# Kernel tuning notes

Measured on AMD Instinct MI355X. Metric: run time of the kernel, lower is better.

Reference implementation:

```python
import jax, jax.numpy as jnp
import numpy as np

# Keras GRUCell (reset_after=True, default in TF2) step
# Keras LSTMCell step (gate order i, f, c, o)
# Keras RNN masking semantics: at masked steps, states are frozen and the
# step output is the previous output (equivalent to freezing every layer's h).

def _gru_step(a, h, W, U, bi, br):
    gx = a @ W + bi          # [B, 3H] input projection
    gh = h @ U + br          # [B, 3H] recurrent projection (reset_after)
    xz, xr, xh = jnp.split(gx, 3, axis=-1)
    rz, rr, rh = jnp.split(gh, 3, axis=-1)
    z = jax.nn.sigmoid(xz + rz)
    r = jax.nn.sigmoid(xr + rr)
    hh = jnp.tanh(xh + r * rh)
    return z * h + (1.0 - z) * hh


def _lstm_step(a, h, c, W, U, b):
    g = a @ W + h @ U + b    # [B, 4H]
    gi, gf, gc, go = jnp.split(g, 4, axis=-1)
    i = jax.nn.sigmoid(gi)
    f = jax.nn.sigmoid(gf)
    cn = f * c + i * jnp.tanh(gc)
    hn = jax.nn.sigmoid(go) * jnp.tanh(cn)
    return hn, cn


def run_gru_stack(x, mask, layers):
    # x: [B,T,D], mask: [B,T] bool; layers: list of (W,U,bi,br)
    B = x.shape[0]
    H = layers[0][1].shape[0]
    xT = jnp.swapaxes(x, 0, 1)      # [T,B,D]
    mT = jnp.swapaxes(mask, 0, 1)   # [T,B]

    def step(hs, inp):
        xt, mt = inp
        a = xt
        new = []
        for (W, U, bi, br), h in zip(layers, hs):
            hn = _gru_step(a, h, W, U, bi, br)
            hn = jnp.where(mt[:, None], hn, h)  # freeze state under mask
            new.append(hn)
            a = hn
        return tuple(new), a

    h0 = tuple(jnp.zeros((B, H), x.dtype) for _ in layers)
    _, ys = jax.lax.scan(step, h0, (xT, mT))
    return jnp.swapaxes(ys, 0, 1)   # [B,T,H]


def run_lstm_stack(x, mask, layers):
    # layers: list of (W,U,b)
    B = x.shape[0]
    H = layers[0][1].shape[0]
    xT = jnp.swapaxes(x, 0, 1)
    mT = jnp.swapaxes(mask, 0, 1)

    def step(state, inp):
        xt, mt = inp
        a = xt
        new = []
        for (W, U, b), (h, c) in zip(layers, state):
            hn, cn = _lstm_step(a, h, c, W, U, b)
            hn = jnp.where(mt[:, None], hn, h)
            cn = jnp.where(mt[:, None], cn, c)
            new.append((hn, cn))
            a = hn
        return tuple(new), a

    s0 = tuple((jnp.zeros((B, H), x.dtype), jnp.zeros((B, H), x.dtype)) for _ in layers)
    _, ys = jax.lax.scan(step, s0, (xT, mT))
    return jnp.swapaxes(ys, 0, 1)


def _forward(x, lengths, g_W0, g_U0, g_bi0, g_br0, g_W1, g_U1, g_bi1, g_br1,
             l_W0, l_U0, l_b0, l_W1, l_U1, l_b1, out_W, out_b):
    T = x.shape[1]
    mask = jnp.arange(T)[None, :] < lengths[:, None]          # [B,T]
    o1 = run_gru_stack(x, mask, [(g_W0, g_U0, g_bi0, g_br0),
                                 (g_W1, g_U1, g_bi1, g_br1)])  # [B,T,H]
    o2 = run_lstm_stack(x, mask, [(l_W0, l_U0, l_b0),
                                  (l_W1, l_U1, l_b1)])          # [B,T,H]
    c = jnp.concatenate([o1, o2], axis=-1)                      # [B,T,2H]
    return c @ out_W + out_b                                    # [B,T,1]


def setup_inputs() -> dict:
    key = jax.random.key(0)
    ks = jax.random.split(key, 16)
    B, T, D, H = 64, 512, 96, 256
    glorot = lambda k, shp: (jax.random.normal(k, shp, dtype=jnp.float32)
                             / np.sqrt(shp[0]).astype(np.float32))
    inp = {
        "x": jax.random.normal(ks[0], (B, T, D), dtype=jnp.float32),
        "lengths": jax.random.randint(ks[1], (B,), 1, T + 1),
        # GRU stack (reset_after: separate input/recurrent biases)
        "g_W0": glorot(ks[2], (D, 3 * H)),
        "g_U0": glorot(ks[3], (H, 3 * H)),
        "g_bi0": jnp.zeros((3 * H,), jnp.float32),
        "g_br0": jnp.zeros((3 * H,), jnp.float32),
        "g_W1": glorot(ks[4], (H, 3 * H)),
        "g_U1": glorot(ks[5], (H, 3 * H)),
        "g_bi1": jnp.zeros((3 * H,), jnp.float32),
        "g_br1": jnp.zeros((3 * H,), jnp.float32),
        # LSTM stack
        "l_W0": glorot(ks[6], (D, 4 * H)),
        "l_U0": glorot(ks[7], (H, 4 * H)),
        "l_b0": jnp.zeros((4 * H,), jnp.float32),
        "l_W1": glorot(ks[8], (H, 4 * H)),
        "l_U1": glorot(ks[9], (H, 4 * H)),
        "l_b1": jnp.zeros((4 * H,), jnp.float32),
        # Dense head on concat [.., 2H] -> 1
        "out_W": glorot(ks[10], (2 * H, 1)),
        "out_b": jnp.zeros((1,), jnp.float32),
    }
    return inp


def reference(x, lengths, g_W0, g_U0, g_bi0, g_br0, g_W1, g_U1, g_bi1, g_br1,
              l_W0, l_U0, l_b0, l_W1, l_U1, l_b1, out_W, out_b):
    return _forward(x, lengths, g_W0, g_U0, g_bi0, g_br0, g_W1, g_U1, g_bi1,
                    g_br1, l_W0, l_U0, l_b0, l_W1, l_U1, l_b1, out_W, out_b)
```

## Files before the change

kernel.cpp:

```cpp
#include <hip/hip_runtime.h>
#include <hip/hip_fp16.h>

constexpr int Tt = 512, Dd = 96, Hh = 256;
constexpr int NS0 = 16;
constexpr int NSP = 8;
typedef unsigned long long u64;

constexpr size_t OFF_P0  = (size_t)4 << 20;
constexpr size_t OFF_P1  = (size_t)12 << 20;
constexpr size_t OFF_FLG = (size_t)20 << 20;
constexpr size_t OFF_W16 = ((size_t)20 << 20) + ((size_t)64 << 10);
constexpr size_t oGW0 = 0;
constexpr size_t oGU0 = oGW0 + (size_t)48 * 768;
constexpr size_t oGW1 = oGU0 + (size_t)128 * 768;
constexpr size_t oGU1 = oGW1 + (size_t)128 * 768;
constexpr size_t oLW0 = oGU1 + (size_t)128 * 768;
constexpr size_t oLU0 = oLW0 + (size_t)48 * 1024;
constexpr size_t oLW1 = oLU0 + (size_t)128 * 1024;
constexpr size_t oLU1 = oLW1 + (size_t)128 * 1024;

__device__ __forceinline__ float sigf(float v) { return 1.0f / (1.0f + __expf(-v)); }
__device__ __forceinline__ u64 agld(const u64* p) {
    return __hip_atomic_load(p, __ATOMIC_RELAXED, __HIP_MEMORY_SCOPE_AGENT);
}
__device__ __forceinline__ int agldi(const int* p) {
    return __hip_atomic_load(p, __ATOMIC_ACQUIRE, __HIP_MEMORY_SCOPE_AGENT);
}
__device__ __forceinline__ void agst(u64* p, u64 v) {
    __hip_atomic_store(p, v, __ATOMIC_RELAXED, __HIP_MEMORY_SCOPE_AGENT);
}

__device__ __forceinline__ float dot2f(unsigned w, unsigned a, float acc) {
#if __has_builtin(__builtin_amdgcn_fdot2)
    typedef _Float16 h2v __attribute__((ext_vector_type(2)));
    h2v wh, ah;
    __builtin_memcpy(&wh, &w, 4);
    __builtin_memcpy(&ah, &a, 4);
    return __builtin_amdgcn_fdot2(wh, ah, acc, false);
#else
    const float2 wf = __half22float2(*(const __half2*)&w);
    const float2 af = __half22float2(*(const __half2*)&a);
    acc = fmaf(wf.x, af.x, acc);
    return fmaf(wf.y, af.y, acc);
#endif
}

__device__ __forceinline__ int hidx(int k, int r) {
    return (k >> 1) * 8 + r * 2 + (k & 1);
}

template<int G>
__device__ __forceinline__ void load4h(uint4* wv, const uint4* __restrict__ M4,
                                       int ldm, int kpb) {
    const int base = (kpb >> 2) * ldm;
    #pragma unroll
    for (int g = 0; g < G; ++g)
        wv[g] = M4[base + g * 256];
}
template<int G>
__device__ __forceinline__ void fma4h(const uint4* wv, const uint4* __restrict__ A4,
                                      int kpb, float4* acc) {
    const uint4 a0 = A4[kpb + 0];
    const uint4 a1 = A4[kpb + 1];
    const uint4 a2 = A4[kpb + 2];
    const uint4 a3 = A4[kpb + 3];
    #pragma unroll
    for (int g = 0; g < G; ++g) {
        const uint4 w = wv[g];
        acc[g].x = dot2f(w.x, a0.x, acc[g].x);
        acc[g].y = dot2f(w.x, a0.y, acc[g].y);
        acc[g].z = dot2f(w.x, a0.z, acc[g].z);
        acc[g].w = dot2f(w.x, a0.w, acc[g].w);
        acc[g].x = dot2f(w.y, a1.x, acc[g].x);
        acc[g].y = dot2f(w.y, a1.y, acc[g].y);
        acc[g].z = dot2f(w.y, a1.z, acc[g].z);
        acc[g].w = dot2f(w.y, a1.w, acc[g].w);
        acc[g].x = dot2f(w.z, a2.x, acc[g].x);
        acc[g].y = dot2f(w.z, a2.y, acc[g].y);
        acc[g].z = dot2f(w.z, a2.z, acc[g].z);
        acc[g].w = dot2f(w.z, a2.w, acc[g].w);
        acc[g].x = dot2f(w.w, a3.x, acc[g].x);
        acc[g].y = dot2f(w.w, a3.y, acc[g].y);
        acc[g].z = dot2f(w.w, a3.z, acc[g].z);
        acc[g].w = dot2f(w.w, a3.w, acc[g].w);
    }
}
template<int G>
__device__ __forceinline__ void gemmP(const uint4* __restrict__ M4, int ldm,
                                      const uint4* __restrict__ A4,
                                      int kp0, int kp1, float4* acc) {
    const int n4 = (kp1 - kp0) >> 2;
    uint4 wv0[G], wv1[G];
    if (n4 <= 0) return;
    load4h<G>(wv0, M4, ldm, kp0);
    int c2 = 0;
    for (; c2 + 2 <= n4; c2 += 2) {
        load4h<G>(wv1, M4, ldm, kp0 + (c2 + 1) * 4);
        fma4h<G>(wv0, A4, kp0 + c2 * 4, acc);
        if (c2 + 2 < n4) load4h<G>(wv0, M4, ldm, kp0 + (c2 + 2) * 4);
        fma4h<G>(wv1, A4, kp0 + (c2 + 1) * 4, acc);
    }
    if (c2 < n4) fma4h<G>(wv0, A4, kp0 + c2 * 4, acc);
}

__global__ void cvt_pair(const float* __restrict__ src, unsigned* __restrict__ dst,
                         int n, int ld) {
    const int i = blockIdx.x * 256 + threadIdx.x;
    if (i >= n) return;
    const int kp = i / ld, col = i - kp * ld;
    const __half2 h = __floats2half2_rn(src[(2 * kp) * ld + col],
                                        src[(2 * kp + 1) * ld + col]);
    dst[((size_t)((kp >> 2) * ld + col) << 2) + (kp & 3)] = *(const unsigned*)&h;
}

__global__ void __launch_bounds__(1024, 4)
rnn_persist(const float* __restrict__ x, const int* __restrict__ lengths,
            const float* __restrict__ gbi0, const float* __restrict__ gbr0,
            const float* __restrict__ gbi1, const float* __restrict__ gbr1,
            const float* __restrict__ lb0, const float* __restrict__ lb1,
            const float* __restrict__ outW, const float* __restrict__ outb,
            float* __restrict__ out, char* __restrict__ wsb)
{
    const int tid = threadIdx.x;
    const int c   = tid & 255;
    const int grp = tid >> 8;
    const int bx  = blockIdx.x;
    const int role  = bx & 3;
    const int chain = (bx >> 2) & 1;
    const int rg    = bx >> 3;
    const int rowbase = rg * 4;

    const int GA  = chain ? 4 : 3;
    const int GAH = GA * Hh;

    u64* h0ring = (u64*)wsb + (size_t)(chain * 16 + rg) * (NS0 * 1024);
    u64* p0ring = (u64*)(wsb + OFF_P0) + (size_t)(chain * 16 + rg) * (NSP * 4096);
    u64* p1ring = (u64*)(wsb + OFF_P1) + (size_t)(chain * 16 + rg) * (NSP * 4096);
    int* flags = (int*)(wsb + OFF_FLG);
    int* flg_r0 = flags + ((chain * 16 + rg) * 4 + 1) * 32;
    int* flg_p1 = flags + ((chain * 16 + rg) * 4 + 2) * 32;
    int* flg_r1 = flags + ((chain * 16 + rg) * 4 + 3) * 32;

    const unsigned* W16 = (const unsigned*)(wsb + OFF_W16);
    size_t woff;
    if (chain == 0) woff = (role == 0) ? oGW0 : (role == 1) ? oGU0 : (role == 2) ? oGW1 : oGU1;
    else            woff = (role == 0) ? oLW0 : (role == 1) ? oLU0 : (role == 2) ? oLW1 : oLU1;
    const uint4* M4 = (const uint4*)(W16 + woff) + c;

    const int KR  = (role == 0) ? Dd : Hh;
    const int KP2 = KR >> 3;
    const int kp0 = grp * KP2, kp1 = kp0 + KP2;

    __shared__ __align__(16) unsigned sAh[128 * 4];
    __shared__ float sG[2 * 4096];
    __shared__ float sRed[16];
    __half* sAhh = (__half*)sAh;
    const uint4* A4 = (const uint4*)sAh;

    const int NP  = 4 * GAH;
    const int npt = NP >> 10;
    float biasv[4];
    int sgidx[4];
    if (role == 0 || role == 2) {
        const float* bsrc = (chain == 0) ? (role == 0 ? gbi0 : gbi1)
                                         : (role == 0 ? lb0 : lb1);
        #pragma unroll
        for (int i = 0; i < 4; ++i) {
            if (i < npt) {
                const int e = tid + i * 1024;
                const int r = e / GAH, rem = e - r * GAH;
                biasv[i] = bsrc[rem];
                sgidx[i] = r * 1024 + rem;
            } else { biasv[i] = 0; sgidx[i] = 0; }
        }
    }
    const int rA = grp;
    const int lenA = lengths[rowbase + rA];
    float brz = 0, brr = 0, brh = 0, ow = 0;
    if (chain == 0 && (role == 1 || role == 3)) {
        const float* br = (role == 1) ? gbr0 : gbr1;
        brz = br[c]; brr = br[Hh + c]; brh = br[2 * Hh + c];
    }
    if (role == 3) ow = outW[chain * Hh + c];
    const float outb0 = outb[0];
    float creg = 0.0f;
    float hprev = 0.0f;

    for (int i = tid; i < 512; i += 1024) sAh[i] = 0;
    __syncthreads();

    for (int t = 0; t < Tt; ++t) {
        if (role == 0) {
            if (t >= NSP) {
                if (tid == 0)
                    while (agldi(flg_r0) < t - NSP + 1) __builtin_amdgcn_s_sleep(1);
                __syncthreads();
            }
            if (tid < 4 * Dd) {
                const int r = tid / Dd, k = tid - r * Dd;
                const float v = x[((size_t)(rowbase + r) * Tt + t) * Dd + k];
                sAhh[hidx(k, r)] = __float2half(v);
            }
            __syncthreads();
        } else if (role == 2) {
            const u64* p0 = h0ring + (size_t)(t & (NS0 - 1)) * 1024 + rA * 256 + c;
            const unsigned want = (unsigned)(t + 1);
            u64 v0;
            do { v0 = agld(p0); } while ((unsigned)v0 != want);
            sAhh[hidx(c, rA)] = __float2half(__uint_as_float((unsigned)(v0 >> 32)));
            __syncthreads();
            if (tid == 0)
                __hip_atomic_exchange(flg_p1, t + 1, __ATOMIC_RELEASE,
                                      __HIP_MEMORY_SCOPE_AGENT);
        }

        if (chain == 0) {
            float4 acc[3] = {{0,0,0,0},{0,0,0,0},{0,0,0,0}};
            gemmP<3>(M4, GAH, A4, kp0, kp1, acc);
            if (grp < 2) {
                #pragma unroll
                for (int g = 0; g < 3; ++g) {
                    sG[grp * 4096 + 0 + g * 256 + c]    = acc[g].x;
                    sG[grp * 4096 + 1024 + g * 256 + c] = acc[g].y;
                    sG[grp * 4096 + 2048 + g * 256 + c] = acc[g].z;
                    sG[grp * 4096 + 3072 + g * 256 + c] = acc[g].w;
                }
            }
            __syncthreads();
            if (grp >= 2) {
                const int b = (grp - 2) * 4096;
                #pragma unroll
                for (int g = 0; g < 3; ++g) {
                    sG[b + 0 + g * 256 + c]    += acc[g].x;
                    sG[b + 1024 + g * 256 + c] += acc[g].y;
                    sG[b + 2048 + g * 256 + c] += acc[g].z;
                    sG[b + 3072 + g * 256 + c] += acc[g].w;
                }
            }
        } else {
            float4 acc[4] = {{0,0,0,0},{0,0,0,0},{0,0,0,0},{0,0,0,0}};
            gemmP<4>(M4, GAH, A4, kp0, kp1, acc);
            if (grp < 2) {
                #pragma unroll
                for (int g = 0; g < 4; ++g) {
                    sG[grp * 4096 + 0 + g * 256 + c]    = acc[g].x;
                    sG[grp * 4096 + 1024 + g * 256 + c] = acc[g].y;
                    sG[grp * 4096 + 2048 + g * 256 + c] = acc[g].z;
                    sG[grp * 4096 + 3072 + g * 256 + c] = acc[g].w;
                }
            }
            __syncthreads();
            if (grp >= 2) {
                const int b = (grp - 2) * 4096;
                #pragma unroll
                for (int g = 0; g < 4; ++g) {
                    sG[b + 0 + g * 256 + c]    += acc[g].x;
                    sG[b + 1024 + g * 256 + c] += acc[g].y;
                    sG[b + 2048 + g * 256 + c] += acc[g].z;
                    sG[b + 3072 + g * 256 + c] += acc[g].w;
                }
            }
        }
        __syncthreads();

        if (role == 0 || role == 2) {
            if (role == 2 && t >= NSP) {
                if (tid == 0)
                    while (agldi(flg_r1) < t - NSP + 1) __builtin_amdgcn_s_sleep(1);
                __syncthreads();
            }
            u64* ring = (role == 0) ? p0ring : p1ring;
            u64* slot = ring + (size_t)(t & (NSP - 1)) * 4096;
            for (int i = 0; i < npt; ++i) {
                const float v = sG[sgidx[i]] + sG[4096 + sgidx[i]] + biasv[i];
                agst(slot + tid + i * 1024,
                     ((u64)__float_as_uint(v) << 32) | (unsigned)(t + 1));
            }
        } else {
            const u64* slot = ((role == 1) ? p0ring : p1ring)
                              + (size_t)(t & (NSP - 1)) * 4096 + rA * GAH + c;
            const unsigned want = (unsigned)(t + 1);
            float P_[4] = {0, 0, 0, 0};
            unsigned dm = 0;
            const unsigned full = (1u << GA) - 1u;
            while (dm != full) {
                #pragma unroll
                for (int g = 0; g < 4; ++g) {
                    if (g < GA && !(dm & (1u << g))) {
                        const u64 v = agld(slot + g * 256);
                        if ((unsigned)v == want) {
                            P_[g] = __uint_as_float((unsigned)(v >> 32));
                            dm |= 1u << g;
                        }
                    }
                }
            }
            if (role == 1 && t >= NS0) {
                if (tid == 0)
                    while (agldi(flg_p1) < t - NS0 + 1) __builtin_amdgcn_s_sleep(1);
                __syncthreads();
            }
            const int r = rA;
            const float hold = hprev;
            float hn;
            if (chain == 0) {
                const float Qz = sG[r * 1024 + c]       + sG[4096 + r * 1024 + c];
                const float Qr = sG[r * 1024 + 256 + c] + sG[4096 + r * 1024 + 256 + c];
                const float Qh = sG[r * 1024 + 512 + c] + sG[4096 + r * 1024 + 512 + c];
                const float z  = sigf(P_[0] + Qz + brz);
                const float rr = sigf(P_[1] + Qr + brr);
                const float hh = tanhf(P_[2] + rr * (Qh + brh));
                hn = z * hold + (1.0f - z) * hh;
                if (t >= lenA) hn = hold;
            } else {
                const float gi = P_[0] + sG[r * 1024 + c]       + sG[4096 + r * 1024 + c];
                const float gf = P_[1] + sG[r * 1024 + 256 + c] + sG[4096 + r * 1024 + 256 + c];
                const float gc = P_[2] + sG[r * 1024 + 512 + c] + sG[4096 + r * 1024 + 512 + c];
                const float go = P_[3] + sG[r * 1024 + 768 + c] + sG[4096 + r * 1024 + 768 + c];
                float cn = sigf(gf) * creg + sigf(gi) * tanhf(gc);
                hn = sigf(go) * tanhf(cn);
                if (t >= lenA) { hn = hold; cn = creg; }
                creg = cn;
            }
            hprev = hn;
            sAhh[hidx(c, r)] = __float2half(hn);
            if (role == 1) {
                agst(h0ring + (size_t)(t & (NS0 - 1)) * 1024 + r * 256 + c,
                     ((u64)__float_as_uint(hn) << 32) | (unsigned)(t + 1));
            } else {
                float vh = hn * ow;
                for (int o = 32; o > 0; o >>= 1)
                    vh += __shfl_down(vh, o);
                if ((tid & 63) == 0) sRed[tid >> 6] = vh;
                __syncthreads();
                if (tid < 4) {
                    const float s = sRed[tid * 4] + sRed[tid * 4 + 1]
                                  + sRed[tid * 4 + 2] + sRed[tid * 4 + 3];
                    atomicAdd(&out[(size_t)(rowbase + tid) * Tt + t],
                              s + (chain ? outb0 : 0.0f));
                }
            }
        }
        __syncthreads();
        if (tid == 0 && (role == 1 || role == 3)) {
            __hip_atomic_exchange((role == 1) ? flg_r0 : flg_r1, t + 1,
                                  __ATOMIC_RELEASE, __HIP_MEMORY_SCOPE_AGENT);
        }
    }
}

extern "C" void kernel_launch(void* const* d_in, const int* in_sizes, int n_in,
                              void* d_out, int out_size, void* d_ws, size_t ws_size,
                              hipStream_t stream) {
    const float* x       = (const float*)d_in[0];
    const int*   lengths = (const int*)d_in[1];
    const float* gW0  = (const float*)d_in[2];
    const float* gU0  = (const float*)d_in[3];
    const float* gbi0 = (const float*)d_in[4];
    const float* gbr0 = (const float*)d_in[5];
    const float* gW1  = (const float*)d_in[6];
    const float* gU1  = (const float*)d_in[7];
    const float* gbi1 = (const float*)d_in[8];
    const float* gbr1 = (const float*)d_in[9];
    const float* lW0  = (const float*)d_in[10];
    const float* lU0  = (const float*)d_in[11];
    const float* lb0  = (const float*)d_in[12];
    const float* lW1  = (const float*)d_in[13];
    const float* lU1  = (const float*)d_in[14];
    const float* lb1  = (const float*)d_in[15];
    const float* outW = (const float*)d_in[16];
    const float* outb = (const float*)d_in[17];
    float* out = (float*)d_out;
    char* wsb  = (char*)d_ws;

    hipMemsetAsync(d_ws, 0, OFF_FLG + (16 << 10), stream);
    hipMemsetAsync(d_out, 0, (size_t)out_size * sizeof(float), stream);

    unsigned* W16 = (unsigned*)(wsb + OFF_W16);
    struct { const float* s; size_t o; int K; int ld; } cv[8] = {
        {gW0, oGW0, 96, 768}, {gU0, oGU0, 256, 768},
        {gW1, oGW1, 256, 768}, {gU1, oGU1, 256, 768},
        {lW0, oLW0, 96, 1024}, {lU0, oLU0, 256, 1024},
        {lW1, oLW1, 256, 1024}, {lU1, oLU1, 256, 1024},
    };
    for (int i = 0; i < 8; ++i) {
        const int n = (cv[i].K / 2) * cv[i].ld;
        cvt_pair<<<(n + 255) / 256, 256, 0, stream>>>(cv[i].s, W16 + cv[i].o, n, cv[i].ld);
    }

    rnn_persist<<<dim3(128), dim3(1024), 0, stream>>>(
        x, lengths, gbi0, gbr0, gbi1, gbr1, lb0, lb1, outW, outb, out, wsb);
}
```

Measured before the change: 4.890 ms.

## Precompute layer-0 input projections in a parallel GEMM, pipeline recurrent roles

Adds a pre-pass that packs x to fp16 and computes the layer-0 input projections (x@W0 plus bias) for all timesteps in a fully parallel kernel, writing them to workspace. A new persistent kernel then runs with three roles per chain instead of four: recurrent layer 0, layer-1 input projection, and recurrent layer 1. This takes the input GEMM off the sequential critical path. The cost is a large fp32 intermediate buffer of roughly 230MB and extra memory traffic. The new path runs only when the workspace is large enough; otherwise the old kernel is used.

New measurement: 6.373 ms. 30.3% more time.

```diff
diff --git a/kernel.cpp b/kernel.cpp
--- a/kernel.cpp
+++ b/kernel.cpp
@@ -18,6 +18,12 @@
 constexpr size_t oLU0 = oLW0 + (size_t)48 * 1024;
 constexpr size_t oLW1 = oLU0 + (size_t)128 * 1024;
 constexpr size_t oLU1 = oLW1 + (size_t)128 * 1024;
+constexpr size_t OFF_XP = (size_t)24 << 20;
+constexpr size_t OFF_PG = (size_t)32 << 20;
+constexpr size_t SZ_PG  = (size_t)64 * 512 * 768 * 4;
+constexpr size_t OFF_PL = OFF_PG + SZ_PG;
+constexpr size_t SZ_PL  = (size_t)64 * 512 * 1024 * 4;
+constexpr size_t WS_NEED = OFF_PL + SZ_PL;
 
 __device__ __forceinline__ float sigf(float v) { return 1.0f / (1.0f + __expf(-v)); }
 __device__ __forceinline__ u64 agld(const u64* p) {
@@ -28,6 +34,9 @@
 }
 __device__ __forceinline__ void agst(u64* p, u64 v) {
     __hip_atomic_store(p, v, __ATOMIC_RELAXED, __HIP_MEMORY_SCOPE_AGENT);
+}
+__device__ __forceinline__ void xrel(int* p, int v) {
+    __hip_atomic_exchange(p, v, __ATOMIC_RELEASE, __HIP_MEMORY_SCOPE_AGENT);
 }
 
 __device__ __forceinline__ float dot2f(unsigned w, unsigned a, float acc) {
@@ -113,6 +122,344 @@
     dst[((size_t)((kp >> 2) * ld + col) << 2) + (kp & 3)] = *(const unsigned*)&h;
 }
 
+__global__ void pack_x(const float* __restrict__ x, unsigned* __restrict__ XP) {
+    const int i = blockIdx.x * 256 + threadIdx.x;
+    if (i >= 64 * Tt * 48) return;
+    const int kp = i % 48;
+    const int bt = i / 48;
+    const __half2 h = __floats2half2_rn(x[(size_t)bt * Dd + 2 * kp],
+                                        x[(size_t)bt * Dd + 2 * kp + 1]);
+    XP[i] = *(const unsigned*)&h;
+}
+
+__global__ void __launch_bounds__(1024, 4)
+gemm_p0(const unsigned* __restrict__ XP, const float* __restrict__ gbi0,
+        const float* __restrict__ lb0, char* __restrict__ wsb)
+{
+    const int tid = threadIdx.x;
+    const int c   = tid & 255;
+    const int grp = tid >> 8;
+    const int bx  = blockIdx.x;
+    const int tt = bx & 31, rg = (bx >> 5) & 15, chain = bx >> 9;
+    const int rowbase = rg * 4;
+    const int GA = chain ? 4 : 3;
+    const int GAH = GA * Hh;
+    const unsigned* W16 = (const unsigned*)(wsb + OFF_W16);
+    const uint4* M4 = (const uint4*)(W16 + (chain ? oLW0 : oGW0)) + c;
+    float* P0 = (float*)(wsb + (chain ? OFF_PL : OFF_PG));
+    const float* bsrc = chain ? lb0 : gbi0;
+
+    __shared__ __align__(16) unsigned sAh[512];
+    __shared__ float sG[2 * 4096];
+    const uint4* A4 = (const uint4*)sAh;
+    const int kp0 = grp * 12, kp1 = kp0 + 12;
+    const int npt = GA;
+    float biasv[4]; int rs[4], remv[4];
+    #pragma unroll
+    for (int i = 0; i < 4; ++i) {
+        if (i < npt) {
+            const int e = tid + i * 1024;
+            const int r = e / GAH, rem = e - r * GAH;
+            biasv[i] = bsrc[rem]; rs[i] = r; remv[i] = rem;
+        } else { biasv[i] = 0; rs[i] = 0; remv[i] = 0; }
+    }
+    for (int t = tt * 16; t < tt * 16 + 16; ++t) {
+        if (tid < 192) {
+            const int row = tid / 48, kp = tid - row * 48;
+            sAh[kp * 4 + row] = XP[((size_t)(rowbase + row) * Tt + t) * 48 + kp];
+        }
+        __syncthreads();
+        if (chain == 0) {
+            float4 acc[3] = {{0,0,0,0},{0,0,0,0},{0,0,0,0}};
+            gemmP<3>(M4, GAH, A4, kp0, kp1, acc);
+            if (grp < 2) {
+                #pragma unroll
+                for (int g = 0; g < 3; ++g) {
+                    sG[grp * 4096 + 0 + g * 256 + c]    = acc[g].x;
+                    sG[grp * 4096 + 1024 + g * 256 + c] = acc[g].y;
+                    sG[grp * 4096 + 2048 + g * 256 + c] = acc[g].z;
+                    sG[grp * 4096 + 3072 + g * 256 + c] = acc[g].w;
+                }
+            }
+            __syncthreads();
+            if (grp >= 2) {
+                const int b = (grp - 2) * 4096;
+                #pragma unroll
+                for (int g = 0; g < 3; ++g) {
+                    sG[b + 0 + g * 256 + c]    += acc[g].x;
+                    sG[b + 1024 + g * 256 + c] += acc[g].y;
+                    sG[b + 2048 + g * 256 + c] += acc[g].z;
+                    sG[b + 3072 + g * 256 + c] += acc[g].w;
+                }
+            }
+        } else {
+            float4 acc[4] = {{0,0,0,0},{0,0,0,0},{0,0,0,0},{0,0,0,0}};
+            gemmP<4>(M4, GAH, A4, kp0, kp1, acc);
+            if (grp < 2) {
+                #pragma unroll
+                for (int g = 0; g < 4; ++g) {
+                    sG[grp * 4096 + 0 + g * 256 + c]    = acc[g].x;
+                    sG[grp * 4096 + 1024 + g * 256 + c] = acc[g].y;
+                    sG[grp * 4096 + 2048 + g * 256 + c] = acc[g].z;
+                    sG[grp * 4096 + 3072 + g * 256 + c] = acc[g].w;
+                }
+            }
+            __syncthreads();
+            if (grp >= 2) {
+                const int b = (grp - 2) * 4096;
+                #pragma unroll
+                for (int g = 0; g < 4; ++g) {
+                    sG[b + 0 + g * 256 + c]    += acc[g].x;
+                    sG[b + 1024 + g * 256 + c] += acc[g].y;
+                    sG[b + 2048 + g * 256 + c] += acc[g].z;
+                    sG[b + 3072 + g * 256 + c] += acc[g].w;
+                }
+            }
+        }
+        __syncthreads();
+        for (int i = 0; i < npt; ++i) {
+            const int idx = rs[i] * 1024 + remv[i];
+            const float v = sG[idx] + sG[4096 + idx] + biasv[i];
+            P0[((size_t)(rowbase + rs[i]) * Tt + t) * GAH + remv[i]] = v;
+        }
+        __syncthreads();
+    }
+}
+
+__global__ void __launch_bounds__(1024, 4)
+rnn_pipe3(const int* __restrict__ lengths, const float* __restrict__ gbr0,
+          const float* __restrict__ gbi1, const float* __restrict__ gbr1,
+          const float* __restrict__ lb1, const float* __restrict__ outW,
+          const float* __restrict__ outb, float* __restrict__ out,
+          char* __restrict__ wsb)
+{
+    const int tid = threadIdx.x;
+    const int c   = tid & 255;
+    const int grp = tid >> 8;
+    const int bx  = blockIdx.x;
+    const int rc = bx & 7, rg = bx >> 3;
+    if (rc >= 6) return;
+    const int chain = rc / 3, role = rc - chain * 3;
+    const int rowbase = rg * 4;
+    const int GA = chain ? 4 : 3;
+    const int GAH = GA * Hh;
+
+    u64* h0ring = (u64*)wsb + (size_t)(chain * 16 + rg) * (NS0 * 1024);
+    u64* p1ring = (u64*)(wsb + OFF_P1) + (size_t)(chain * 16 + rg) * (NSP * 4096);
+    int* flags = (int*)(wsb + OFF_FLG);
+    int* flg_p1 = flags + ((chain * 16 + rg) * 4 + 2) * 32;
+    int* flg_r1 = flags + ((chain * 16 + rg) * 4 + 3) * 32;
+
+    const unsigned* W16 = (const unsigned*)(wsb + OFF_W16);
+    const size_t woff = (chain == 0)
+        ? (role == 0 ? oGU0 : role == 1 ? oGW1 : oGU1)
+        : (role == 0 ? oLU0 : role == 1 ? oLW1 : oLU1);
+    const uint4* M4 = (const uint4*)(W16 + woff) + c;
+    const float* P0 = (const float*)(wsb + (chain ? OFF_PL : OFF_PG));
+
+    const int KP2 = Hh >> 3;
+    const int kp0 = grp * KP2, kp1 = kp0 + KP2;
+
+    __shared__ __align__(16) unsigned sAh[128 * 4];
+    __shared__ float sG[2 * 4096];
+    __shared__ float sRed[16];
+    __half* sAhh = (__half*)sAh;
+    const uint4* A4 = (const uint4*)sAh;
+
+    const int npt = GA;
+    float biasv[4]; int sgidx[4];
+    if (role == 1) {
+        const float* bsrc = chain ? lb1 : gbi1;
+        #pragma unroll
+        for (int i = 0; i < 4; ++i) {
+            if (i < npt) {
+                const int e = tid + i * 1024;
+                const int r = e / GAH, rem = e - r * GAH;
+                biasv[i] = bsrc[rem];
+                sgidx[i] = r * 1024 + rem;
+            } else { biasv[i] = 0; sgidx[i] = 0; }
+        }
+    }
+    const int rA = grp;
+    const int lenA = lengths[rowbase + rA];
+    float brz = 0, brr = 0, brh = 0, ow = 0;
+    if (chain == 0 && (role == 0 || role == 2)) {
+        const float* br = (role == 0) ? gbr0 : gbr1;
+        brz = br[c]; brr = br[Hh + c]; brh = br[2 * Hh + c];
+    }
+    if (role == 2) ow = outW[chain * Hh + c];
+    const float outb0 = outb[0];
+    float creg = 0.0f, hprev = 0.0f;
+
+    for (int i = tid; i < 512; i += 1024) sAh[i] = 0;
+    __syncthreads();
+
+    for (int t = 0; t < Tt; ++t) {
+        float p0r[4] = {0, 0, 0, 0};
+        u64 pr[4];
+        if (role == 0) {
+            if (t >= NS0) {
+                if (tid == 0)
+                    while (agldi(flg_p1) < t - NS0 + 1) __builtin_amdgcn_s_sleep(1);
+                __syncthreads();
+            }
+            const size_t pb = ((size_t)(rowbase + rA) * Tt + t) * GAH + c;
+            #pragma unroll
+            for (int g = 0; g < 4; ++g)
+                if (g < GA) p0r[g] = P0[pb + g * 256];
+        } else if (role == 1) {
+            const u64* pw = h0ring + (size_t)(t & (NS0 - 1)) * 1024 + rA * 256 + c;
+            const unsigned want = (unsigned)(t + 1);
+            u64 v;
+            do { v = agld(pw); } while ((unsigned)v != want);
+            sAhh[hidx(c, rA)] = __float2half(__uint_as_float((unsigned)(v >> 32)));
+            __syncthreads();
+            if (tid == 0) xrel(flg_p1, t + 1);
+        } else {
+            const u64* slot = p1ring + (size_t)(t & (NSP - 1)) * 4096 + rA * GAH + c;
+            #pragma unroll
+            for (int g = 0; g < 4; ++g)
+                if (g < GA) pr[g] = agld(slot + g * 256);
+        }
+
+        if (chain == 0) {
+            float4 acc[3] = {{0,0,0,0},{0,0,0,0},{0,0,0,0}};
+            gemmP<3>(M4, GAH, A4, kp0, kp1, acc);
+            if (grp < 2) {
+                #pragma unroll
+                for (int g = 0; g < 3; ++g) {
+                    sG[grp * 4096 + 0 + g * 256 + c]    = acc[g].x;
+                    sG[grp * 4096 + 1024 + g * 256 + c] = acc[g].y;
+                    sG[grp * 4096 + 2048 + g * 256 + c] = acc[g].z;
+                    sG[grp * 4096 + 3072 + g * 256 + c] = acc[g].w;
+                }
+            }
+            __syncthreads();
+            if (grp >= 2) {
+                const int b = (grp - 2) * 4096;
+                #pragma unroll
+                for (int g = 0; g < 3; ++g) {
+                    sG[b + 0 + g * 256 + c]    += acc[g].x;
+                    sG[b + 1024 + g * 256 + c] += acc[g].y;
+                    sG[b + 2048 + g * 256 + c] += acc[g].z;
+                    sG[b + 3072 + g * 256 + c] += acc[g].w;
+                }
+            }
+        } else {
+            float4 acc[4] = {{0,0,0,0},{0,0,0,0},{0,0,0,0},{0,0,0,0}};
+            gemmP<4>(M4, GAH, A4, kp0, kp1, acc);
+            if (grp < 2) {
+                #pragma unroll
+                for (int g = 0; g < 4; ++g) {
+                    sG[grp * 4096 + 0 + g * 256 + c]    = acc[g].x;
+                    sG[grp * 4096 + 1024 + g * 256 + c] = acc[g].y;
+                    sG[grp * 4096 + 2048 + g * 256 + c] = acc[g].z;
+                    sG[grp * 4096 + 3072 + g * 256 + c] = acc[g].w;
+                }
+            }
+            __syncthreads();
+            if (grp >= 2) {
+                const int b = (grp - 2) * 4096;
+                #pragma unroll
+                for (int g = 0; g < 4; ++g) {
+                    sG[b + 0 + g * 256 + c]    += acc[g].x;
+                    sG[b + 1024 + g * 256 + c] += acc[g].y;
+                    sG[b + 2048 + g * 256 + c] += acc[g].z;
+                    sG[b + 3072 + g * 256 + c] += acc[g].w;
+                }
+            }
+        }
+        __syncthreads();
+
+        if (role == 0) {
+            const int r = rA;
+            const float Qz = sG[r * 1024 + c]       + sG[4096 + r * 1024 + c];
+            const float Qr = sG[r * 1024 + 256 + c] + sG[4096 + r * 1024 + 256 + c];
+            const float Qh = sG[r * 1024 + 512 + c] + sG[4096 + r * 1024 + 512 + c];
+            const float hold = hprev;
+            float hn;
+            if (chain == 0) {
+                const float z  = sigf(p0r[0] + Qz + brz);
+                const float rr = sigf(p0r[1] + Qr + brr);
+                const float hh = tanhf(p0r[2] + rr * (Qh + brh));
+                hn = z * hold + (1.0f - z) * hh;
+                if (t >= lenA) hn = hold;
+            } else {
+                const float Qo = sG[r * 1024 + 768 + c] + sG[4096 + r * 1024 + 768 + c];
+                float cn = sigf(p0r[1] + Qr) * creg + sigf(p0r[0] + Qz) * tanhf(p0r[2] + Qh);
+                hn = sigf(p0r[3] + Qo) * tanhf(cn);
+                if (t >= lenA) { hn = hold; cn = creg; }
+                creg = cn;
+            }
+            hprev = hn;
+            sAhh[hidx(c, r)] = __float2half(hn);
+            agst(h0ring + (size_t)(t & (NS0 - 1)) * 1024 + r * 256 + c,
+                 ((u64)__float_as_uint(hn) << 32) | (unsigned)(t + 1));
+        } else if (role == 1) {
+            if (t >= NSP) {
+                if (tid == 0)
+                    while (agldi(flg_r1) < t - NSP + 1) __builtin_amdgcn_s_sleep(1);
+                __syncthreads();
+            }
+            u64* slot = p1ring + (size_t)(t & (NSP - 1)) * 4096;
+            for (int i = 0; i < npt; ++i) {
+                const float v = sG[sgidx[i]] + sG[4096 + sgidx[i]] + biasv[i];
+                agst(slot + tid + i * 1024,
+                     ((u64)__float_as_uint(v) << 32) | (unsigned)(t + 1));
+            }
+        } else {
+            const u64* slot = p1ring + (size_t)(t & (NSP - 1)) * 4096 + rA * GAH + c;
+            const unsigned want = (unsigned)(t + 1);
+            float P_[4] = {0, 0, 0, 0};
+            #pragma unroll
+            for (int g = 0; g < 4; ++g) {
+                if (g < GA) {
+                    u64 v = pr[g];
+                    while ((unsigned)v != want) v = agld(slot + g * 256);
+                    P_[g] = __uint_as_float((unsigned)(v >> 32));
+                }
+            }
+            const int r = rA;
+            const float hold = hprev;
+            float hn;
+            if (chain == 0) {
+                const float Qz = sG[r * 1024 + c]       + sG[4096 + r * 1024 + c];
+                const float Qr = sG[r * 1024 + 256 + c] + sG[4096 + r * 1024 + 256 + c];
+                const float Qh = sG[r * 1024 + 512 + c] + sG[4096 + r * 1024 + 512 + c];
+                const float z  = sigf(P_[0] + Qz + brz);
+                const float rr = sigf(P_[1] + Qr + brr);
+                const float hh = tanhf(P_[2] + rr * (Qh + brh));
+                hn = z * hold + (1.0f - z) * hh;
+                if (t >= lenA) hn = hold;
+            } else {
+                const float gi = P_[0] + sG[r * 1024 + c]       + sG[4096 + r * 1024 + c];
+                const float gf = P_[1] + sG[r * 1024 + 256 + c] + sG[4096 + r * 1024 + 256 + c];
+                const float gc = P_[2] + sG[r * 1024 + 512 + c] + sG[4096 + r * 1024 + 512 + c];
+                const float go = P_[3] + sG[r * 1024 + 768 + c] + sG[4096 + r * 1024 + 768 + c];
+                float cn = sigf(gf) * creg + sigf(gi) * tanhf(gc);
+                hn = sigf(go) * tanhf(cn);
+                if (t >= lenA) { hn = hold; cn = creg; }
+                creg = cn;
+            }
+            hprev = hn;
+            sAhh[hidx(c, r)] = __float2half(hn);
+            float vh = hn * ow;
+            for (int o = 32; o > 0; o >>= 1)
+                vh += __shfl_down(vh, o);
+            if ((tid & 63) == 0) sRed[tid >> 6] = vh;
+            __syncthreads();
+            if (tid < 4) {
+                const float s = sRed[tid * 4] + sRed[tid * 4 + 1]
+                              + sRed[tid * 4 + 2] + sRed[tid * 4 + 3];
+                atomicAdd(&out[(size_t)(rowbase + tid) * Tt + t],
+                          s + (chain ? outb0 : 0.0f));
+            }
+        }
+        __syncthreads();
+        if (tid == 0 && role == 2) xrel(flg_r1, t + 1);
+    }
+}
+
 __global__ void __launch_bounds__(1024, 4)
 rnn_persist(const float* __restrict__ x, const int* __restrict__ lengths,
             const float* __restrict__ gbi0, const float* __restrict__ gbr0,
@@ -388,6 +735,15 @@
         cvt_pair<<<(n + 255) / 256, 256, 0, stream>>>(cv[i].s, W16 + cv[i].o, n, cv[i].ld);
     }
 
-    rnn_persist<<<dim3(128), dim3(1024), 0, stream>>>(
-        x, lengths, gbi0, gbr0, gbi1, gbr1, lb0, lb1, outW, outb, out, wsb);
-}
+    if (ws_size >= WS_NEED) {
+        unsigned* XP = (unsigned*)(wsb + OFF_XP);
+        const int nxp = 64 * Tt * 48;
+        pack_x<<<(nxp + 255) / 256, 256, 0, stream>>>(x, XP);
+        gemm_p0<<<dim3(1024), dim3(1024), 0, stream>>>(XP, gbi0, lb0, wsb);
+        rnn_pipe3<<<dim3(128), dim3(1024), 0, stream>>>(
+            lengths, gbr0, gbi1, gbr1, lb1, outW, outb, out, wsb);
+    } else {
+        rnn_persist<<<dim3(128), dim3(1024), 0, stream>>>(
+            x, lengths, gbi0, gbr0, gbi1, gbr1, lb0, lb1, outW, outb, out, wsb);
+    }
+}
```

## Split recurrent and layer-1 input roles across two blocks per column half

Applied to the files above, without the earlier changes.

Each row-group now uses seven blocks instead of four. The input-projection block for layer 0 stays as before, while the recurrent and layer-1 input roles are split into two blocks that each own half of the hidden columns. The two halves of each recurrent layer swap their h values through a new ring buffer each step, and new flags track progress per half. The aim is to halve the serial per-step GEMM and update work on the critical recurrent path. The cost is more blocks (224), more cross-block polling, and finer synchronization that adds latency to every step.

Measured after the change: 12.41 ms. 154% more time.

```diff
diff --git a/kernel.cpp b/kernel.cpp
--- a/kernel.cpp
+++ b/kernel.cpp
@@ -3,13 +3,16 @@
 
 constexpr int Tt = 512, Dd = 96, Hh = 256;
 constexpr int NS0 = 16;
+constexpr int NS1 = 16;
 constexpr int NSP = 8;
 typedef unsigned long long u64;
 
+constexpr size_t OFF_H0  = 0;
 constexpr size_t OFF_P0  = (size_t)4 << 20;
 constexpr size_t OFF_P1  = (size_t)12 << 20;
-constexpr size_t OFF_FLG = (size_t)20 << 20;
-constexpr size_t OFF_W16 = ((size_t)20 << 20) + ((size_t)64 << 10);
+constexpr size_t OFF_H1  = (size_t)20 << 20;
+constexpr size_t OFF_FLG = (size_t)24 << 20;
+constexpr size_t OFF_W16 = ((size_t)24 << 20) + ((size_t)64 << 10);
 constexpr size_t oGW0 = 0;
 constexpr size_t oGU0 = oGW0 + (size_t)48 * 768;
 constexpr size_t oGW1 = oGU0 + (size_t)128 * 768;
@@ -28,6 +31,14 @@
 }
 __device__ __forceinline__ void agst(u64* p, u64 v) {
     __hip_atomic_store(p, v, __ATOMIC_RELAXED, __HIP_MEMORY_SCOPE_AGENT);
+}
+__device__ __forceinline__ void xrel(int* p, int v) {
+    __hip_atomic_exchange(p, v, __ATOMIC_RELEASE, __HIP_MEMORY_SCOPE_AGENT);
+}
+__device__ __forceinline__ float pollF(const u64* p, unsigned want) {
+    u64 v = agld(p);
+    while ((unsigned)v != want) v = agld(p);
+    return __uint_as_float((unsigned)(v >> 32));
 }
 
 __device__ __forceinline__ float dot2f(unsigned w, unsigned a, float acc) {
@@ -114,239 +125,348 @@
 }
 
 __global__ void __launch_bounds__(1024, 4)
-rnn_persist(const float* __restrict__ x, const int* __restrict__ lengths,
-            const float* __restrict__ gbi0, const float* __restrict__ gbr0,
-            const float* __restrict__ gbi1, const float* __restrict__ gbr1,
-            const float* __restrict__ lb0, const float* __restrict__ lb1,
-            const float* __restrict__ outW, const float* __restrict__ outb,
-            float* __restrict__ out, char* __restrict__ wsb)
+rnn_split(const float* __restrict__ x, const int* __restrict__ lengths,
+          const float* __restrict__ gbi0, const float* __restrict__ gbr0,
+          const float* __restrict__ gbi1, const float* __restrict__ gbr1,
+          const float* __restrict__ lb0, const float* __restrict__ lb1,
+          const float* __restrict__ outW, const float* __restrict__ outb,
+          float* __restrict__ out, char* __restrict__ wsb)
 {
     const int tid = threadIdx.x;
-    const int c   = tid & 255;
-    const int grp = tid >> 8;
     const int bx  = blockIdx.x;
-    const int role  = bx & 3;
-    const int chain = (bx >> 2) & 1;
-    const int rg    = bx >> 3;
+    const int grpid = bx / 7;
+    const int sub   = bx - grpid * 7;
+    const int chain = grpid >> 4;
+    const int rg    = grpid & 15;
     const int rowbase = rg * 4;
+    const int kind = (sub == 0) ? 0 : 1 + ((sub - 1) >> 1);
+    const int half = (sub == 0) ? 0 : ((sub - 1) & 1);
 
     const int GA  = chain ? 4 : 3;
     const int GAH = GA * Hh;
-
-    u64* h0ring = (u64*)wsb + (size_t)(chain * 16 + rg) * (NS0 * 1024);
-    u64* p0ring = (u64*)(wsb + OFF_P0) + (size_t)(chain * 16 + rg) * (NSP * 4096);
-    u64* p1ring = (u64*)(wsb + OFF_P1) + (size_t)(chain * 16 + rg) * (NSP * 4096);
-    int* flags = (int*)(wsb + OFF_FLG);
-    int* flg_r0 = flags + ((chain * 16 + rg) * 4 + 1) * 32;
-    int* flg_p1 = flags + ((chain * 16 + rg) * 4 + 2) * 32;
-    int* flg_r1 = flags + ((chain * 16 + rg) * 4 + 3) * 32;
+    const int RS  = GA * 128;
+
+    u64* h0ring = (u64*)(wsb + OFF_H0) + (size_t)grpid * (NS0 * 1024);
+    u64* p0ring = (u64*)(wsb + OFF_P0) + (size_t)grpid * (NSP * 4096);
+    u64* p1ring = (u64*)(wsb + OFF_P1) + (size_t)grpid * (NSP * 4096);
+    u64* h1ring = (u64*)(wsb + OFF_H1) + (size_t)grpid * (NS1 * 1024);
+    int* flg = (int*)(wsb + OFF_FLG) + grpid * (16 * 32);
+    #define F(i) (flg + (i) * 32)
 
     const unsigned* W16 = (const unsigned*)(wsb + OFF_W16);
     size_t woff;
-    if (chain == 0) woff = (role == 0) ? oGW0 : (role == 1) ? oGU0 : (role == 2) ? oGW1 : oGU1;
-    else            woff = (role == 0) ? oLW0 : (role == 1) ? oLU0 : (role == 2) ? oLW1 : oLU1;
-    const uint4* M4 = (const uint4*)(W16 + woff) + c;
-
-    const int KR  = (role == 0) ? Dd : Hh;
-    const int KP2 = KR >> 3;
-    const int kp0 = grp * KP2, kp1 = kp0 + KP2;
+    if (chain == 0) woff = (kind == 0) ? oGW0 : (kind == 1) ? oGU0 : (kind == 2) ? oGW1 : oGU1;
+    else            woff = (kind == 0) ? oLW0 : (kind == 1) ? oLU0 : (kind == 2) ? oLW1 : oLU1;
+    const int c256 = tid & 255, c128 = tid & 127;
+    const int grp4 = tid >> 8, grp8 = tid >> 7;
+    const uint4* M4 = (const uint4*)(W16 + woff)
+                      + ((kind == 0) ? c256 : (half * 128 + c128));
+    const int kp0 = (kind == 0) ? grp4 * 12 : grp8 * 16;
+    const int kp1 = kp0 + ((kind == 0) ? 12 : 16);
 
     __shared__ __align__(16) unsigned sAh[128 * 4];
-    __shared__ float sG[2 * 4096];
+    __shared__ float sG[8192];
     __shared__ float sRed[16];
     __half* sAhh = (__half*)sAh;
     const uint4* A4 = (const uint4*)sAh;
 
-    const int NP  = 4 * GAH;
-    const int npt = NP >> 10;
-    float biasv[4];
-    int sgidx[4];
-    if (role == 0 || role == 2) {
-        const float* bsrc = (chain == 0) ? (role == 0 ? gbi0 : gbi1)
-                                         : (role == 0 ? lb0 : lb1);
+    const int NP = 4 * GAH;
+    const int npt0 = NP >> 10;
+    float biasv[4]; int sgidx[4], ringoff[4];
+    if (kind == 0) {
+        const float* bsrc = chain ? lb0 : gbi0;
         #pragma unroll
         for (int i = 0; i < 4; ++i) {
-            if (i < npt) {
+            if (i < npt0) {
                 const int e = tid + i * 1024;
                 const int r = e / GAH, rem = e - r * GAH;
-                biasv[i] = bsrc[rem];
-                sgidx[i] = r * 1024 + rem;
-            } else { biasv[i] = 0; sgidx[i] = 0; }
+                biasv[i] = bsrc[rem]; sgidx[i] = r * 1024 + rem; ringoff[i] = e;
+            } else { biasv[i] = 0; sgidx[i] = 0; ringoff[i] = 0; }
+        }
+    } else if (kind == 2) {
+        const float* bsrc = chain ? lb1 : gbi1;
+        const int NPh = 4 * GA * 128;
+        #pragma unroll
+        for (int i = 0; i < 2; ++i) {
+            const int e = tid + i * 1024;
+            if (e < NPh) {
+                const int u = e & 127, rest = e >> 7;
+                const int r = rest / GA, g = rest - r * GA;
+                biasv[i]   = bsrc[g * 256 + half * 128 + u];
+                sgidx[i]   = r * RS + g * 128 + u;
+                ringoff[i] = r * GAH + g * 256 + half * 128 + u;
+            } else { biasv[i] = 0; sgidx[i] = -1; ringoff[i] = 0; }
         }
     }
-    const int rA = grp;
-    const int lenA = lengths[rowbase + rA];
+
+    const int uu = tid & 127, urow = (tid >> 7) & 3;
+    const bool upd = (kind == 1 || kind == 3) && tid < 512;
+    const int ucol = half * 128 + uu;
+    int len = Tt + 1;
     float brz = 0, brr = 0, brh = 0, ow = 0;
-    if (chain == 0 && (role == 1 || role == 3)) {
-        const float* br = (role == 1) ? gbr0 : gbr1;
-        brz = br[c]; brr = br[Hh + c]; brh = br[2 * Hh + c];
+    if (upd) {
+        len = lengths[rowbase + urow];
+        if (chain == 0) {
+            const float* br = (kind == 1) ? gbr0 : gbr1;
+            brz = br[ucol]; brr = br[256 + ucol]; brh = br[512 + ucol];
+        }
+        if (kind == 3) ow = outW[chain * Hh + ucol];
     }
-    if (role == 3) ow = outW[chain * Hh + c];
     const float outb0 = outb[0];
-    float creg = 0.0f;
-    float hprev = 0.0f;
+    float creg = 0.0f, hprev = 0.0f;
 
     for (int i = tid; i < 512; i += 1024) sAh[i] = 0;
     __syncthreads();
 
     for (int t = 0; t < Tt; ++t) {
-        if (role == 0) {
+        if (kind == 0) {
             if (t >= NSP) {
                 if (tid == 0)
-                    while (agldi(flg_r0) < t - NSP + 1) __builtin_amdgcn_s_sleep(1);
+                    while (min(agldi(F(0)), agldi(F(1))) < t - NSP + 1)
+                        __builtin_amdgcn_s_sleep(1);
                 __syncthreads();
             }
             if (tid < 4 * Dd) {
                 const int r = tid / Dd, k = tid - r * Dd;
-                const float v = x[((size_t)(rowbase + r) * Tt + t) * Dd + k];
-                sAhh[hidx(k, r)] = __float2half(v);
+                sAhh[hidx(k, r)] =
+                    __float2half(x[((size_t)(rowbase + r) * Tt + t) * Dd + k]);
             }
             __syncthreads();
-        } else if (role == 2) {
-            const u64* p0 = h0ring + (size_t)(t & (NS0 - 1)) * 1024 + rA * 256 + c;
-            const unsigned want = (unsigned)(t + 1);
-            u64 v0;
-            do { v0 = agld(p0); } while ((unsigned)v0 != want);
-            sAhh[hidx(c, rA)] = __float2half(__uint_as_float((unsigned)(v0 >> 32)));
+        } else if (kind == 1 || kind == 3) {
+            if (t > 0 && tid < 512) {
+                const u64* ring = (kind == 1) ? h0ring : h1ring;
+                const u64* base = ring + (size_t)((t - 1) & (NS0 - 1)) * 1024;
+                const int k = (1 - half) * 128 + uu;
+                const float v = pollF(base + urow * 256 + k, (unsigned)t);
+                sAhh[hidx(k, urow)] = __float2half(v);
+            }
             __syncthreads();
-            if (tid == 0)
-                __hip_atomic_exchange(flg_p1, t + 1, __ATOMIC_RELEASE,
-                                      __HIP_MEMORY_SCOPE_AGENT);
-        }
-
-        if (chain == 0) {
-            float4 acc[3] = {{0,0,0,0},{0,0,0,0},{0,0,0,0}};
-            gemmP<3>(M4, GAH, A4, kp0, kp1, acc);
-            if (grp < 2) {
+        } else {
+            const int un = tid & 255, r = tid >> 8;
+            const float v = pollF(h0ring + (size_t)(t & (NS0 - 1)) * 1024 + r * 256 + un,
+                                  (unsigned)(t + 1));
+            sAhh[hidx(un, r)] = __float2half(v);
+            __syncthreads();
+            if (tid == 0) xrel(F(2 + half), t + 1);
+        }
+
+        if (kind == 0) {
+            if (chain == 0) {
+                float4 acc[3] = {{0,0,0,0},{0,0,0,0},{0,0,0,0}};
+                gemmP<3>(M4, GAH, A4, kp0, kp1, acc);
+                if (grp4 < 2) {
+                    #pragma unroll
+                    for (int g = 0; g < 3; ++g) {
+                        sG[grp4 * 4096 + 0 + g * 256 + c256]    = acc[g].x;
+                        sG[grp4 * 4096 + 1024 + g * 256 + c256] = acc[g].y;
+                        sG[grp4 * 4096 + 2048 + g * 256 + c256] = acc[g].z;
+                        sG[grp4 * 4096 + 3072 + g * 256 + c256] = acc[g].w;
+                    }
+                }
+                __syncthreads();
+                if (grp4 >= 2) {
+                    const int b = (grp4 - 2) * 4096;
+                    #pragma unroll
+                    for (int g = 0; g < 3; ++g) {
+                        sG[b + 0 + g * 256 + c256]    += acc[g].x;
+                        sG[b + 1024 + g * 256 + c256] += acc[g].y;
+                        sG[b + 2048 + g * 256 + c256] += acc[g].z;
+                        sG[b + 3072 + g * 256 + c256] += acc[g].w;
+                    }
+                }
+            } else {
+                float4 acc[4] = {{0,0,0,0},{0,0,0,0},{0,0,0,0},{0,0,0,0}};
+                gemmP<4>(M4, GAH, A4, kp0, kp1, acc);
+                if (grp4 < 2) {
+                    #pragma unroll
+                    for (int g = 0; g < 4; ++g) {
+                        sG[grp4 * 4096 + 0 + g * 256 + c256]    = acc[g].x;
+                        sG[grp4 * 4096 + 1024 + g * 256 + c256] = acc[g].y;
+                        sG[grp4 * 4096 + 2048 + g * 256 + c256] = acc[g].z;
+                        sG[grp4 * 4096 + 3072 + g * 256 + c256] = acc[g].w;
+                    }
+                }
+                __syncthreads();
+                if (grp4 >= 2) {
+                    const int b = (grp4 - 2) * 4096;
+                    #pragma unroll
+                    for (int g = 0; g < 4; ++g) {
+                        sG[b + 0 + g * 256 + c256]    += acc[g].x;
+                        sG[b + 1024 + g * 256 + c256] += acc[g].y;
+                        sG[b + 2048 + g * 256 + c256] += acc[g].z;
+                        sG[b + 3072 + g * 256 + c256] += acc[g].w;
+                    }
+                }
+            }
+        } else {
+            if (chain == 0) {
+                float4 acc[3] = {{0,0,0,0},{0,0,0,0},{0,0,0,0}};
+                gemmP<3>(M4, GAH, A4, kp0, kp1, acc);
+                if (grp8 < 4) {
+                    const int b = grp8 * 2048;
+                    #pragma unroll
+                    for (int g = 0; g < 3; ++g) {
+                        sG[b + 0 * RS + g * 128 + c128] = acc[g].x;
+                        sG[b + 1 * RS + g * 128 + c128] = acc[g].y;
+                        sG[b + 2 * RS + g * 128 + c128] = acc[g].z;
+                        sG[b + 3 * RS + g * 128 + c128] = acc[g].w;
+                    }
+                }
+                __syncthreads();
+                if (grp8 >= 4) {
+                    const int b = (grp8 - 4) * 2048;
+                    #pragma unroll
+                    for (int g = 0; g < 3; ++g) {
+                        sG[b + 0 * RS + g * 128 + c128] += acc[g].x;
+                        sG[b + 1 * RS + g * 128 + c128] += acc[g].y;
+                        sG[b + 2 * RS + g * 128 + c128] += acc[g].z;
+                        sG[b + 3 * RS + g * 128 + c128] += acc[g].w;
+                    }
+                }
+            } else {
+                float4 acc[4] = {{0,0,0,0},{0,0,0,0},{0,0,0,0},{0,0,0,0}};
+                gemmP<4>(M4, GAH, A4, kp0, kp1, acc);
+                if (grp8 < 4) {
+                    const int b = grp8 * 2048;
+                    #pragma unroll
+                    for (int g = 0; g < 4; ++g) {
+                        sG[b + 0 * RS + g * 128 + c128] = acc[g].x;
+                        sG[b + 1 * RS + g * 128 + c128] = acc[g].y;
+                        sG[b + 2 * RS + g * 128 + c128] = acc[g].z;
+                        sG[b + 3 * RS + g * 128 + c128] = acc[g].w;
+                    }
+                }
+                __syncthreads();
+                if (grp8 >= 4) {
+                    const int b = (grp8 - 4) * 2048;
+                    #pragma unroll
+                    for (int g = 0; g < 4; ++g) {
+                        sG[b + 0 * RS + g * 128 + c128] += acc[g].x;
+                        sG[b + 1 * RS + g * 128 + c128] += acc[g].y;
+                        sG[b + 2 * RS + g * 128 + c128] += acc[g].z;
+                        sG[b + 3 * RS + g * 128 + c128] += acc[g].w;
+                    }
+                }
+            }
+        }
+        __syncthreads();
+
+        if (kind == 0) {
+            u64* slot = p0ring + (size_t)(t & (NSP - 1)) * 4096;
+            for (int i = 0; i < npt0; ++i) {
+                const float v = sG[sgidx[i]] + sG[4096 + sgidx[i]] + biasv[i];
+                agst(slot + ringoff[i],
+                     ((u64)__float_as_uint(v) << 32) | (unsigned)(t + 1));
+            }
+        } else if (kind == 2) {
+            if (t >= NSP) {
+                if (tid == 0)
+                    while (min(agldi(F(6)), agldi(F(7))) < t - NSP + 1)
+                        __builtin_amdgcn_s_sleep(1);
+                __syncthreads();
+            }
+            u64* slot = p1ring + (size_t)(t & (NSP - 1)) * 4096;
+            #pragma unroll
+            for (int i = 0; i < 2; ++i) {
+                if (sgidx[i] >= 0) {
+                    const float v = sG[sgidx[i]] + sG[2048 + sgidx[i]]
+                                  + sG[4096 + sgidx[i]] + sG[6144 + sgidx[i]] + biasv[i];
+                    agst(slot + ringoff[i],
+                         ((u64)__float_as_uint(v) << 32) | (unsigned)(t + 1));
+                }
+            }
+        } else {
+            float hn = 0.0f, vh = 0.0f;
+            if (upd) {
+                const u64* slot = ((kind == 1) ? p0ring : p1ring)
+                                  + (size_t)(t & (NSP - 1)) * 4096 + urow * GAH + ucol;
+                const unsigned want = (unsigned)(t + 1);
+                float P_[4] = {0, 0, 0, 0};
+                unsigned dm = 0;
+                const unsigned full = (1u << GA) - 1u;
+                while (dm != full) {
+                    #pragma unroll
+                    for (int g = 0; g < 4; ++g) {
+                        if (g < GA && !(dm & (1u << g))) {
+                            const u64 v = agld(slot + g * 256);
+                            if ((unsigned)v == want) {
+                                P_[g] = __uint_as_float((unsigned)(v >> 32));
+                                dm |= 1u << g;
+                            }
+                        }
+                    }
+                }
+                const int qb = urow * RS + uu;
+                float Q[4] = {0, 0, 0, 0};
                 #pragma unroll
-                for (int g = 0; g < 3; ++g) {
-                    sG[grp * 4096 + 0 + g * 256 + c]    = acc[g].x;
-                    sG[grp * 4096 + 1024 + g * 256 + c] = acc[g].y;
-                    sG[grp * 4096 + 2048 + g * 256 + c] = acc[g].z;
-                    sG[grp * 4096 + 3072 + g * 256 + c] = acc[g].w;
-                }
-            }
-            __syncthreads();
-            if (grp >= 2) {
-                const int b = (grp - 2) * 4096;
-                #pragma unroll
-                for (int g = 0; g < 3; ++g) {
-                    sG[b + 0 + g * 256 + c]    += acc[g].x;
-                    sG[b + 1024 + g * 256 + c] += acc[g].y;
-                    sG[b + 2048 + g * 256 + c] += acc[g].z;
-                    sG[b + 3072 + g * 256 + c] += acc[g].w;
-                }
-            }
-        } else {
-            float4 acc[4] = {{0,0,0,0},{0,0,0,0},{0,0,0,0},{0,0,0,0}};
-            gemmP<4>(M4, GAH, A4, kp0, kp1, acc);
-            if (grp < 2) {
-                #pragma unroll
-                for (int g = 0; g < 4; ++g) {
-                    sG[grp * 4096 + 0 + g * 256 + c]    = acc[g].x;
-                    sG[grp * 4096 + 1024 + g * 256 + c] = acc[g].y;
-                    sG[grp * 4096 + 2048 + g * 256 + c] = acc[g].z;
-                    sG[grp * 4096 + 3072 + g * 256 + c] = acc[g].w;
-                }
-            }
-            __syncthreads();
-            if (grp >= 2) {
-                const int b = (grp - 2) * 4096;
-                #pragma unroll
-                for (int g = 0; g < 4; ++g) {
-                    sG[b + 0 + g * 256 + c]    += acc[g].x;
-                    sG[b + 1024 + g * 256 + c] += acc[g].y;
-                    sG[b + 2048 + g * 256 + c] += acc[g].z;
-                    sG[b + 3072 + g * 256 + c] += acc[g].w;
-                }
+                for (int g = 0; g < 4; ++g)
+                    if (g < GA)
+                        Q[g] = sG[qb + g * 128] + sG[2048 + qb + g * 128]
+                             + sG[4096 + qb + g * 128] + sG[6144 + qb + g * 128];
+                const float hold = hprev;
+                if (chain == 0) {
+                    const float z  = sigf(P_[0] + Q[0] + brz);
+                    const float r_ = sigf(P_[1] + Q[1] + brr);
+                    const float hh = tanhf(P_[2] + r_ * (Q[2] + brh));
+                    hn = z * hold + (1.0f - z) * hh;
+                    if (t >= len) hn = hold;
+                } else {
+                    float cn = sigf(P_[1] + Q[1]) * creg
+                             + sigf(P_[0] + Q[0]) * tanhf(P_[2] + Q[2]);
+                    hn = sigf(P_[3] + Q[3]) * tanhf(cn);
+                    if (t >= len) { hn = hold; cn = creg; }
+                    creg = cn;
+                }
+                hprev = hn;
+                sAhh[hidx(ucol, urow)] = __float2half(hn);
+                if (kind == 3) vh = hn * ow;
+            }
+            if (kind == 3) {
+                if (upd) {
+                    #pragma unroll
+                    for (int o = 32; o > 0; o >>= 1) vh += __shfl_down(vh, o);
+                    if ((tid & 63) == 0) sRed[tid >> 6] = vh;
+                }
+                __syncthreads();
+                if (tid < 4) {
+                    const float s = sRed[2 * tid] + sRed[2 * tid + 1];
+                    atomicAdd(&out[(size_t)(rowbase + tid) * Tt + t],
+                              s + ((chain == 1 && half == 0) ? outb0 : 0.0f));
+                }
+            }
+            const int NSH = (kind == 1) ? NS0 : NS1;
+            if (t >= NSH) {
+                if (tid == 0) {
+                    int need = t - NSH + 1;
+                    if (kind == 1) {
+                        while (min(min(agldi(F(2)), agldi(F(3))),
+                                   min(agldi(F(4)), agldi(F(5)))) < need)
+                            __builtin_amdgcn_s_sleep(1);
+                    } else {
+                        while (min(agldi(F(8)), agldi(F(9))) < need)
+                            __builtin_amdgcn_s_sleep(1);
+                    }
+                }
+                __syncthreads();
+            }
+            if (upd) {
+                u64* ring = (kind == 1) ? h0ring : h1ring;
+                agst(ring + (size_t)(t & (NS0 - 1)) * 1024 + urow * 256 + ucol,
+                     ((u64)__float_as_uint(hn) << 32) | (unsigned)(t + 1));
             }
         }
         __syncthreads();
-
-        if (role == 0 || role == 2) {
-            if (role == 2 && t >= NSP) {
-                if (tid == 0)
-                    while (agldi(flg_r1) < t - NSP + 1) __builtin_amdgcn_s_sleep(1);
-                __syncthreads();
-            }
-            u64* ring = (role == 0) ? p0ring : p1ring;
-            u64* slot = ring + (size_t)(t & (NSP - 1)) * 4096;
-            for (int i = 0; i < npt; ++i) {
-                const float v = sG[sgidx[i]] + sG[4096 + sgidx[i]] + biasv[i];
-                agst(slot + tid + i * 1024,
-                     ((u64)__float_as_uint(v) << 32) | (unsigned)(t + 1));
-            }
-        } else {
-            const u64* slot = ((role == 1) ? p0ring : p1ring)
-                              + (size_t)(t & (NSP - 1)) * 4096 + rA * GAH + c;
-            const unsigned want = (unsigned)(t + 1);
-            float P_[4] = {0, 0, 0, 0};
-            unsigned dm = 0;
-            const unsigned full = (1u << GA) - 1u;
-            while (dm != full) {
-                #pragma unroll
-                for (int g = 0; g < 4; ++g) {
-                    if (g < GA && !(dm & (1u << g))) {
-                        const u64 v = agld(slot + g * 256);
-                        if ((unsigned)v == want) {
-                            P_[g] = __uint_as_float((unsigned)(v >> 32));
-                            dm |= 1u << g;
-                        }
-                    }
-                }
-            }
-            if (role == 1 && t >= NS0) {
-                if (tid == 0)
-                    while (agldi(flg_p1) < t - NS0 + 1) __builtin_amdgcn_s_sleep(1);
-                __syncthreads();
-            }
-            const int r = rA;
-            const float hold = hprev;
-            float hn;
-            if (chain == 0) {
-                const float Qz = sG[r * 1024 + c]       + sG[4096 + r * 1024 + c];
-                const float Qr = sG[r * 1024 + 256 + c] + sG[4096 + r * 1024 + 256 + c];
-                const float Qh = sG[r * 1024 + 512 + c] + sG[4096 + r * 1024 + 512 + c];
-                const float z  = sigf(P_[0] + Qz + brz);
-                const float rr = sigf(P_[1] + Qr + brr);
-                const float hh = tanhf(P_[2] + rr * (Qh + brh));
-                hn = z * hold + (1.0f - z) * hh;
-                if (t >= lenA) hn = hold;
-            } else {
-                const float gi = P_[0] + sG[r * 1024 + c]       + sG[4096 + r * 1024 + c];
-                const float gf = P_[1] + sG[r * 1024 + 256 + c] + sG[4096 + r * 1024 + 256 + c];
-                const float gc = P_[2] + sG[r * 1024 + 512 + c] + sG[4096 + r * 1024 + 512 + c];
-                const float go = P_[3] + sG[r * 1024 + 768 + c] + sG[4096 + r * 1024 + 768 + c];
-                float cn = sigf(gf) * creg + sigf(gi) * tanhf(gc);
-                hn = sigf(go) * tanhf(cn);
-                if (t >= lenA) { hn = hold; cn = creg; }
-                creg = cn;
-            }
-            hprev = hn;
-            sAhh[hidx(c, r)] = __float2half(hn);
-            if (role == 1) {
-                agst(h0ring + (size_t)(t & (NS0 - 1)) * 1024 + r * 256 + c,
-                     ((u64)__float_as_uint(hn) << 32) | (unsigned)(t + 1));
-            } else {
-                float vh = hn * ow;
-                for (int o = 32; o > 0; o >>= 1)
-                    vh += __shfl_down(vh, o);
-                if ((tid & 63) == 0) sRed[tid >> 6] = vh;
-                __syncthreads();
-                if (tid < 4) {
-                    const float s = sRed[tid * 4] + sRed[tid * 4 + 1]
-                                  + sRed[tid * 4 + 2] + sRed[tid * 4 + 3];
-                    atomicAdd(&out[(size_t)(rowbase + tid) * Tt + t],
-                              s + (chain ? outb0 : 0.0f));
-                }
-            }
-        }
-        __syncthreads();
-        if (tid == 0 && (role == 1 || role == 3)) {
-            __hip_atomic_exchange((role == 1) ? flg_r0 : flg_r1, t + 1,
-                                  __ATOMIC_RELEASE, __HIP_MEMORY_SCOPE_AGENT);
+        if (tid == 0) {
+            if (kind == 1) {
+                xrel(F(0 + half), t + 1);
+                xrel(F(4 + half), t);
+            } else if (kind == 3) {
+                xrel(F(6 + half), t + 1);
+                xrel(F(8 + half), t);
+            }
         }
     }
+    #undef F
 }
 
 extern "C" void kernel_launch(void* const* d_in, const int* in_sizes, int n_in,
@@ -373,7 +493,7 @@
     float* out = (float*)d_out;
     char* wsb  = (char*)d_ws;
 
-    hipMemsetAsync(d_ws, 0, OFF_FLG + (16 << 10), stream);
+    hipMemsetAsync(d_ws, 0, OFF_W16, stream);
     hipMemsetAsync(d_out, 0, (size_t)out_size * sizeof(float), stream);
 
     unsigned* W16 = (unsigned*)(wsb + OFF_W16);
@@ -388,6 +508,6 @@
         cvt_pair<<<(n + 255) / 256, 256, 0, stream>>>(cv[i].s, W16 + cv[i].o, n, cv[i].ld);
     }
 
-    rnn_persist<<<dim3(128), dim3(1024), 0, stream>>>(
+    rnn_split<<<dim3(224), dim3(1024), 0, stream>>>(
         x, lengths, gbi0, gbr0, gbi1, gbr1, lb0, lb1, outW, outb, out, wsb);
 }
```
